# Kernel tuning notes

Measured on AMD Instinct MI355X. Metric: run time of the kernel, lower is better.

## Reference

```python
import jax, jax.numpy as jnp
import numpy as np

B, T, F = 128, 512, 16   # batch, seq len, n_features
K, PAD, H = 5, 2, 32     # conv kernel, padding, per-feature GRU hidden
NEG = 0.01               # LeakyReLU default negative slope


def setup_inputs() -> dict:
    key = jax.random.key(0)
    ks = iter(jax.random.split(key, 64))

    def u(shape, fan):
        s = 1.0 / np.sqrt(fan)
        return jax.random.uniform(next(ks), shape, jnp.float32, -s, s)

    inp = {}
    inp['x'] = jax.random.normal(next(ks), (B, 2, T), jnp.float32)
    # gru_enc: input=2, hidden=F, unidirectional (torch layout: W_ih [3H,I], W_hh [3H,H])
    inp['enc_Wih'] = u((3 * F, 2), F)
    inp['enc_Whh'] = u((3 * F, F), F)
    inp['enc_bih'] = u((3 * F,), F)
    inp['enc_bhh'] = u((3 * F,), F)
    # last_layers_gru (per feature): input=1, hidden=H, bidirectional
    for d in ('f', 'b'):
        inp[f'g1_Wih_{d}'] = u((F, 3 * H, 1), H)
        inp[f'g1_Whh_{d}'] = u((F, 3 * H, H), H)
        inp[f'g1_bih_{d}'] = u((F, 3 * H), H)
        inp[f'g1_bhh_{d}'] = u((F, 3 * H), H)
    # layers_gru (per feature): input=2H, hidden=H, unidirectional
    inp['g2_Wih'] = u((F, 3 * H, 2 * H), H)
    inp['g2_Whh'] = u((F, 3 * H, H), H)
    inp['g2_bih'] = u((F, 3 * H), H)
    inp['g2_bhh'] = u((F, 3 * H), H)
    # ConvTranspose1d weights, torch layout [C_in, C_out, K]
    inp['w3'] = u((F, 32, 64, K), 32 * K)
    inp['b3'] = u((F, 64), 32 * K)
    inp['w2'] = u((F, 64, 128, K), 64 * K)
    inp['b2'] = u((F, 128), 64 * K)
    inp['w1'] = u((F, 128, 1, K), 128 * K)
    inp['b1'] = u((F, 1), 128 * K)
    return inp


def gru(x, Wih, Whh, bih, bhh):
    # x: [B, T, I] -> [B, T, H]; torch GRU cell math
    Hh = Whh.shape[1]
    xp = jnp.einsum('bti,gi->btg', x, Wih) + bih  # [B,T,3H], input proj for all t

    def step(h, xt):
        g = h @ Whh.T + bhh
        xr, xz, xn = jnp.split(xt, 3, -1)
        hr, hz, hn = jnp.split(g, 3, -1)
        r = jax.nn.sigmoid(xr + hr)
        z = jax.nn.sigmoid(xz + hz)
        n = jnp.tanh(xn + r * hn)
        h = (1 - z) * n + z * h
        return h, h

    h0 = jnp.zeros((x.shape[0], Hh), x.dtype)
    _, ys = jax.lax.scan(step, h0, jnp.swapaxes(xp, 0, 1))
    return jnp.swapaxes(ys, 0, 1)


def bigru(x, Wf, Hf, bif, bhf, Wb, Hb, bib, bhb):
    fwd = gru(x, Wf, Hf, bif, bhf)
    bwd = gru(x[:, ::-1], Wb, Hb, bib, bhb)[:, ::-1]
    return jnp.concatenate([fwd, bwd], -1)


def convT(x, w, b):
    # ConvTranspose1d(stride=1, padding=PAD): x [B,Cin,T], w [Cin,Cout,K]
    wc = jnp.flip(w, -1).transpose(1, 0, 2)  # -> [Cout,Cin,K] cross-correlation kernel
    y = jax.lax.conv_general_dilated(
        x, wc, (1,), [(K - 1 - PAD, K - 1 - PAD)],
        dimension_numbers=('NCH', 'OIH', 'NCH'))
    return y + b[None, :, None]


def reference(x, enc_Wih, enc_Whh, enc_bih, enc_bhh,
              g1_Wih_f, g1_Whh_f, g1_bih_f, g1_bhh_f,
              g1_Wih_b, g1_Whh_b, g1_bih_b, g1_bhh_b,
              g2_Wih, g2_Whh, g2_bih, g2_bhh,
              w3, b3, w2, b2, w1, b1):
    leaky = lambda v: jnp.where(v >= 0, v, NEG * v)
    # encoder GRU over time: x [B,2,T] -> [B,T,F]
    h = gru(jnp.swapaxes(x, 1, 2), enc_Wih, enc_Whh, enc_bih, enc_bhh)

    def per_feature(xi, W1f, H1f, bi1f, bh1f, W1b, H1b, bi1b, bh1b,
                    W2, H2, bi2, bh2, w3_, b3_, w2_, b2_, w1_, b1_):
        # xi: [B,T] single feature channel
        u = bigru(xi[..., None], W1f, H1f, bi1f, bh1f, W1b, H1b, bi1b, bh1b)  # [B,T,2H]
        u = gru(u, W2, H2, bi2, bh2)        # [B,T,H]
        u = jnp.swapaxes(u, 1, 2)           # [B,H,T]
        u = leaky(convT(u, w3_, b3_))       # [B,64,T]
        u = leaky(convT(u, w2_, b2_))       # [B,128,T]
        u = leaky(convT(u, w1_, b1_))       # [B,1,T]
        return u[:, 0]                      # [B,T]

    feats = jnp.moveaxis(h, 2, 0)           # [F,B,T]
    out = jax.vmap(per_feature)(feats,
                                g1_Wih_f, g1_Whh_f, g1_bih_f, g1_bhh_f,
                                g1_Wih_b, g1_Whh_b, g1_bih_b, g1_bhh_b,
                                g2_Wih, g2_Whh, g2_bih, g2_bhh,
                                w3, b3, w2, b2, w1, b1)  # [F,B,T]
    return jnp.moveaxis(out, 0, 2)          # [B,T,F]
```

## Files before the change

kernel.cpp:

```cpp
#include <hip/hip_runtime.h>
#include <math.h>

#define BB 128
#define TT 512
#define FF 16

typedef _Float16 half8 __attribute__((ext_vector_type(8)));
typedef float floatx4 __attribute__((ext_vector_type(4)));

union HU { uint4 u; half8 h; };

__device__ __forceinline__ float bf2f(unsigned short u){
  union { unsigned int i; float f; } c; c.i = ((unsigned int)u) << 16; return c.f;
}
__device__ __forceinline__ unsigned short f2bf(float f){
  union { float f; unsigned int i; } c; c.f = f;
  unsigned int x = c.i;
  unsigned int r = (x + 0x7fffu + ((x >> 16) & 1u)) >> 16;
  return (unsigned short)r;
}
__device__ __forceinline__ float sigm(float x){
  return __builtin_amdgcn_rcpf(1.f + __expf(-x));
}
__device__ __forceinline__ float tanh_fast(float x){
  x = fminf(15.f, fmaxf(-15.f, x));
  float e = __expf(-2.f*x);
  return (1.f - e)*__builtin_amdgcn_rcpf(1.f + e);
}
__device__ __forceinline__ float lrelu(float v){ return v >= 0.f ? v : 0.01f*v; }

__device__ __forceinline__ unsigned int packhl(float v){
  _Float16 hh = (_Float16)v;
  float hf = (float)hh;
  _Float16 hl = (_Float16)(v - hf);
  union { _Float16 h; unsigned short s; } a, b;
  a.h = hh; b.h = hl;
  return (unsigned int)a.s | ((unsigned int)b.s << 16);
}

__device__ __forceinline__ void unpackAB(uint4 P0, uint4 P1, HU& Ah, HU& Al){
  Ah.u.x = (P0.x & 0xffffu) | (P0.y << 16);
  Ah.u.y = (P0.z & 0xffffu) | (P0.w << 16);
  Ah.u.z = (P1.x & 0xffffu) | (P1.y << 16);
  Ah.u.w = (P1.z & 0xffffu) | (P1.w << 16);
  Al.u.x = (P0.x >> 16) | (P0.y & 0xffff0000u);
  Al.u.y = (P0.z >> 16) | (P0.w & 0xffff0000u);
  Al.u.z = (P1.x >> 16) | (P1.y & 0xffff0000u);
  Al.u.w = (P1.z >> 16) | (P1.w & 0xffff0000u);
}

#define MFMA16(A,B,C) __builtin_amdgcn_mfma_f32_16x16x32_f16((A),(B),(C),0,0,0)

__global__ __launch_bounds__(256) void fill_kernel(unsigned short* out, int n, float v){
  int i = blockIdx.x*256 + threadIdx.x;
  if (i < n) out[i] = f2bf(v);
}

__global__ __launch_bounds__(256) void detect1_kernel(const unsigned short* x, float* maxbuf){
  __shared__ float red[256];
  const int base = blockIdx.x*4096 + threadIdx.x*16;
  const uint4* p = (const uint4*)(x + base);
  uint4 a = p[0], b = p[1];
  unsigned int ws[8] = {a.x,a.y,a.z,a.w,b.x,b.y,b.z,b.w};
  float m = 0.f;
  #pragma unroll
  for (int i=0;i<8;i++){
    float v0 = fabsf(bf2f((unsigned short)(ws[i] & 0xffffu)));
    float v1 = fabsf(bf2f((unsigned short)(ws[i] >> 16)));
    if (!isfinite(v0)) v0 = 3e38f;
    if (!isfinite(v1)) v1 = 3e38f;
    m = fmaxf(m, fmaxf(v0, v1));
  }
  red[threadIdx.x] = m; __syncthreads();
  for (int s=128; s>0; s>>=1){
    if (threadIdx.x < s) red[threadIdx.x] = fmaxf(red[threadIdx.x], red[threadIdx.x+s]);
    __syncthreads();
  }
  if (threadIdx.x == 0) maxbuf[blockIdx.x] = red[0];
}
__global__ __launch_bounds__(64) void detect2_kernel(const float* maxbuf, int* flag){
  if (threadIdx.x == 0){
    float m = 0.f;
    for (int i=0;i<32;i++) m = fmaxf(m, maxbuf[i]);
    *flag = (m < 1e4f) ? 1 : 0;
  }
}

struct CvtArgs { const void* p[23]; int sz[23]; int ofs[23]; };

__global__ __launch_bounds__(256) void convert_kernel(CvtArgs a, const int* flag, float* dst){
  const int i = blockIdx.x;
  const int n = a.sz[i];
  const int start = blockIdx.y * 16384;
  if (start >= n) return;
  const int end = (start + 16384 < n) ? start + 16384 : n;
  float* d = dst + a.ofs[i];
  const int s4 = start >> 2, e4 = end >> 2;
  if (*flag){
    const unsigned short* s = (const unsigned short*)a.p[i];
    for (int e = s4 + threadIdx.x; e < e4; e += 256){
      uint2 w = *(const uint2*)(s + 4*e);
      float4 o;
      o.x = bf2f((unsigned short)(w.x & 0xffffu));
      o.y = bf2f((unsigned short)(w.x >> 16));
      o.z = bf2f((unsigned short)(w.y & 0xffffu));
      o.w = bf2f((unsigned short)(w.y >> 16));
      *(float4*)(d + 4*e) = o;
    }
  } else {
    const float* s = (const float*)a.p[i];
    for (int e = s4 + threadIdx.x; e < e4; e += 256)
      *(float4*)(d + 4*e) = *(const float4*)(s + 4*e);
  }
}

__global__ __launch_bounds__(256) void prep16_kernel(
    const float* __restrict__ cvt, _Float16* __restrict__ h16,
    int o6, int o10, int o14, int o13, int o17, int o19, int o2)
{
  const int i = blockIdx.x*256 + threadIdx.x;
  const int y = blockIdx.y;
  if (y == 0){ if (i < 49152) h16[i]          = (_Float16)cvt[o6  + i]; }
  else if (y == 1){ if (i < 49152) h16[49152 + i]  = (_Float16)cvt[o10 + i]; }
  else if (y == 2){ if (i < 49152) h16[98304 + i]  = (_Float16)cvt[o14 + i]; }
  else if (y == 3){ if (i < 98304) h16[147456 + i] = (_Float16)cvt[o13 + i]; }
  else if (y == 4){
    if (i < 163840){
      int ci = i & 31, co = (i >> 5) & 63, fj = i >> 11;
      int f = fj / 5, j = fj - 5*f;
      h16[245760 + i] = (_Float16)cvt[o17 + ((f*32 + ci)*64 + co)*5 + j];
    }
  } else if (y == 5){
    if (i < 655360){
      int ci = i & 63, co = (i >> 6) & 127, fj = i >> 13;
      int f = fj / 5, j = fj - 5*f;
      h16[409600 + i] = (_Float16)cvt[o19 + ((f*64 + ci)*128 + co)*5 + j];
    }
  } else {
    if (i < 1536){
      int k = i & 31, row = i >> 5;
      h16[1064960 + i] = (k < 16) ? (_Float16)cvt[o2 + row*16 + k] : (_Float16)0.f;
    }
  }
}

__global__ __launch_bounds__(128) void xt_kernel(const float* __restrict__ cvt, float* __restrict__ xTp){
  const int t = blockIdx.x, b = threadIdx.x;
  xTp[t*BB + b]            = cvt[(b*2 + 0)*TT + t];
  xTp[65536 + t*BB + b]    = cvt[(b*2 + 1)*TT + t];
}

__global__ __launch_bounds__(64) void enc_kernel(
    const float* __restrict__ xTp, const _Float16* __restrict__ whhE,
    const float* __restrict__ Wih, const float* __restrict__ bih,
    const float* __restrict__ bhh, float* __restrict__ xfeatT)
{
  const int b0 = blockIdx.x*16;
  const int l = threadIdx.x, ml = l & 15, q = l >> 4;
  __shared__ unsigned int Hpk[2][16][20];
  half8 Bw[3];
  #pragma unroll
  for (int c=0;c<3;c++)
    Bw[c] = *(const half8*)(whhE + (16*c + ml)*32 + 8*q);
  float w0r=Wih[ml*2],      w1r=Wih[ml*2+1],      bir=bih[ml],    bhr=bhh[ml];
  float w0z=Wih[(16+ml)*2], w1z=Wih[(16+ml)*2+1], biz=bih[16+ml], bhz=bhh[16+ml];
  float w0n=Wih[(32+ml)*2], w1n=Wih[(32+ml)*2+1], bin_=bih[32+ml], bhn=bhh[32+ml];
  float hm[4] = {0,0,0,0};
  HU Ah, Al; Ah.u = make_uint4(0,0,0,0); Al.u = Ah.u;
  const floatx4 z4 = {0.f,0.f,0.f,0.f};
  int pp = 0;
  floatx4 x0v = *(const floatx4*)(xTp + b0 + 4*q);
  floatx4 x1v = *(const floatx4*)(xTp + 65536 + b0 + 4*q);
  for (int t=0;t<TT;t++){
    const int tn = (t < 511) ? t+1 : t;
    floatx4 x0n = *(const floatx4*)(xTp + tn*BB + b0 + 4*q);
    floatx4 x1n = *(const floatx4*)(xTp + 65536 + tn*BB + b0 + 4*q);
    floatx4 C[3];
    #pragma unroll
    for (int c=0;c<3;c++){
      C[c] = MFMA16(Al.h, Bw[c], z4);
      C[c] = MFMA16(Ah.h, Bw[c], C[c]);
    }
    #pragma unroll
    for (int r=0;r<4;r++){
      float xb0 = x0v[r], xb1 = x1v[r];
      float rr = sigm(fmaf(w0r,xb0,fmaf(w1r,xb1,bir)) + C[0][r] + bhr);
      float zz = sigm(fmaf(w0z,xb0,fmaf(w1z,xb1,biz)) + C[1][r] + bhz);
      float nn = tanh_fast(fmaf(w0n,xb0,fmaf(w1n,xb1,bin_)) + rr*(C[2][r] + bhn));
      float hn = nn + zz*(hm[r] - nn);
      hm[r] = hn;
      Hpk[pp][4*q + r][ml] = packhl(hn);
      xfeatT[((size_t)ml*TT + t)*BB + b0 + 4*q + r] = hn;
    }
    __syncthreads();
    if (q < 2){
      uint4 P0 = *(const uint4*)&Hpk[pp][ml][8*q];
      uint4 P1 = *(const uint4*)&Hpk[pp][ml][8*q + 4];
      unpackAB(P0, P1, Ah, Al);
    } else { Ah.u = make_uint4(0,0,0,0); Al.u = Ah.u; }
    pp ^= 1;
    x0v = x0n; x1v = x1n;
  }
}

__global__ __launch_bounds__(128) void g1b_kernel(
    const float* __restrict__ xT, const _Float16* __restrict__ whh_h,
    const float* __restrict__ wih, const float* __restrict__ bih,
    const float* __restrict__ bhh, _Float16* __restrict__ trace)
{
  const int f = blockIdx.x, b0 = blockIdx.y*16;
  const int wid = threadIdx.x >> 6, l = threadIdx.x & 63, ml = l & 15, q = l >> 4;
  __shared__ unsigned int Hpk[2][16][36];
  half8 Bw[3];
  #pragma unroll
  for (int i=0;i<3;i++){
    int tc = 2*i + wid;
    Bw[i] = *(const half8*)(whh_h + (size_t)f*3072 + (16*tc + ml)*32 + 8*q);
  }
  const int j = 16*wid + ml, base = f*96;
  float wir=wih[base+j], wiz=wih[base+32+j], win=wih[base+64+j];
  float br_=bih[base+j]+bhh[base+j];
  float bz_=bih[base+32+j]+bhh[base+32+j];
  float bin_=bih[base+64+j], bhn_=bhh[base+64+j];
  float hm[4] = {0,0,0,0};
  HU Ah, Al; Ah.u = make_uint4(0,0,0,0); Al.u = Ah.u;
  const floatx4 z4 = {0.f,0.f,0.f,0.f};
  int pp = 0;
  floatx4 xv = *(const floatx4*)(xT + ((size_t)f*TT + 511)*BB + b0 + 4*q);
  const int dostore = (wid == (q >> 1));
  for (int s=0;s<512;s++){
    const int t = 511 - s;
    const int tn = (s < 511) ? t-1 : t;
    floatx4 xnx = *(const floatx4*)(xT + ((size_t)f*TT + tn)*BB + b0 + 4*q);
    floatx4 C[3];
    #pragma unroll
    for (int i=0;i<3;i++){
      C[i] = MFMA16(Al.h, Bw[i], z4);
      C[i] = MFMA16(Ah.h, Bw[i], C[i]);
    }
    #pragma unroll
    for (int r=0;r<4;r++){
      float xb = xv[r];
      float rr = sigm(fmaf(wir, xb, br_) + C[0][r]);
      float zz = sigm(fmaf(wiz, xb, bz_) + C[1][r]);
      float nn = tanh_fast(fmaf(win, xb, bin_) + rr*(C[2][r] + bhn_));
      float hn = nn + zz*(hm[r] - nn);
      hm[r] = hn;
      Hpk[pp][4*q + r][j] = packhl(hn);
    }
    __syncthreads();
    {
      uint4 P0 = *(const uint4*)&Hpk[pp][ml][8*q];
      uint4 P1 = *(const uint4*)&Hpk[pp][ml][8*q + 4];
      unpackAB(P0, P1, Ah, Al);
    }
    if (dostore)
      *(uint4*)(trace + (((size_t)(f*BB + b0 + ml))*TT + t)*32 + 8*q) = Ah.u;
    pp ^= 1;
    xv = xnx;
  }
}

__global__ __launch_bounds__(128) void g1bf_kernel(
    const float* __restrict__ xT,
    const _Float16* __restrict__ whhB_h, const float* __restrict__ wihB,
    const float* __restrict__ bihB, const float* __restrict__ bhhB,
    const _Float16* __restrict__ whhF_h, const float* __restrict__ wihF,
    const float* __restrict__ bihF, const float* __restrict__ bhhF,
    _Float16* __restrict__ traceB, _Float16* __restrict__ traceF)
{
  const int f = blockIdx.x, b0 = blockIdx.y*16, dir = blockIdx.z;
  const _Float16* whh_h = dir ? whhF_h : whhB_h;
  const float* wih = dir ? wihF : wihB;
  const float* bih = dir ? bihF : bihB;
  const float* bhh = dir ? bhhF : bhhB;
  _Float16* trace = dir ? traceF : traceB;
  const int wid = threadIdx.x >> 6, l = threadIdx.x & 63, ml = l & 15, q = l >> 4;
  __shared__ unsigned int Hpk[2][16][36];
  half8 Bw[3];
  #pragma unroll
  for (int i=0;i<3;i++){
    int tc = 2*i + wid;
    Bw[i] = *(const half8*)(whh_h + (size_t)f*3072 + (16*tc + ml)*32 + 8*q);
  }
  const int j = 16*wid + ml, base = f*96;
  float wir=wih[base+j], wiz=wih[base+32+j], win=wih[base+64+j];
  float br_=bih[base+j]+bhh[base+j];
  float bz_=bih[base+32+j]+bhh[base+32+j];
  float bin_=bih[base+64+j], bhn_=bhh[base+64+j];
  float hm[4] = {0,0,0,0};
  HU Ah, Al; Ah.u = make_uint4(0,0,0,0); Al.u = Ah.u;
  const floatx4 z4 = {0.f,0.f,0.f,0.f};
  int pp = 0;
  const int tfirst = dir ? 0 : 511;
  floatx4 xv = *(const floatx4*)(xT + ((size_t)f*TT + tfirst)*BB + b0 + 4*q);
  const int dostore = (wid == (q >> 1));
  for (int s=0;s<512;s++){
    const int t  = dir ? s : 511 - s;
    const int sn = (s < 511) ? s+1 : s;
    const int tn = dir ? sn : 511 - sn;
    floatx4 xnx = *(const floatx4*)(xT + ((size_t)f*TT + tn)*BB + b0 + 4*q);
    floatx4 C[3];
    #pragma unroll
    for (int i=0;i<3;i++){
      C[i] = MFMA16(Al.h, Bw[i], z4);
      C[i] = MFMA16(Ah.h, Bw[i], C[i]);
    }
    #pragma unroll
    for (int r=0;r<4;r++){
      float xb = xv[r];
      float rr = sigm(fmaf(wir, xb, br_) + C[0][r]);
      float zz = sigm(fmaf(wiz, xb, bz_) + C[1][r]);
      float nn = tanh_fast(fmaf(win, xb, bin_) + rr*(C[2][r] + bhn_));
      float hn = nn + zz*(hm[r] - nn);
      hm[r] = hn;
      Hpk[pp][4*q + r][j] = packhl(hn);
    }
    __syncthreads();
    {
      uint4 P0 = *(const uint4*)&Hpk[pp][ml][8*q];
      uint4 P1 = *(const uint4*)&Hpk[pp][ml][8*q + 4];
      unpackAB(P0, P1, Ah, Al);
    }
    if (dostore)
      *(uint4*)(trace + (((size_t)(f*BB + b0 + ml))*TT + t)*32 + 8*q) = Ah.u;
    pp ^= 1;
    xv = xnx;
  }
}

__global__ __launch_bounds__(128) void g2_kernel(
    const float* __restrict__ xT,
    const _Float16* __restrict__ wh1_h, const float* __restrict__ wih1,
    const float* __restrict__ bih1, const float* __restrict__ bhh1,
    const _Float16* __restrict__ wh2_h, const _Float16* __restrict__ w2i_h,
    const float* __restrict__ bih2, const float* __restrict__ bhh2,
    _Float16* __restrict__ trace)
{
  const int f = blockIdx.x, b0 = blockIdx.y*16;
  const int wid = threadIdx.x >> 6, l = threadIdx.x & 63, ml = l & 15, q = l >> 4;
  __shared__ unsigned int Hpk1[2][16][36];
  __shared__ unsigned int Hpk2[2][16][36];
  half8 B1[3], Bh2[3], Bx0[3], Bx1[3];
  #pragma unroll
  for (int i=0;i<3;i++){
    int tc = 2*i + wid;
    B1[i]  = *(const half8*)(wh1_h + (size_t)f*3072 + (16*tc + ml)*32 + 8*q);
    Bh2[i] = *(const half8*)(wh2_h + (size_t)f*3072 + (16*tc + ml)*32 + 8*q);
    Bx0[i] = *(const half8*)(w2i_h + (size_t)f*6144 + (16*tc + ml)*64 + 8*q);
    Bx1[i] = *(const half8*)(w2i_h + (size_t)f*6144 + (16*tc + ml)*64 + 32 + 8*q);
  }
  const int j = 16*wid + ml, base = f*96;
  float wir=wih1[base+j], wiz=wih1[base+32+j], win=wih1[base+64+j];
  float br1_=bih1[base+j]+bhh1[base+j];
  float bz1_=bih1[base+32+j]+bhh1[base+32+j];
  float bin1_=bih1[base+64+j], bhn1_=bhh1[base+64+j];
  float br2_=bih2[base+j]+bhh2[base+j];
  float bz2_=bih2[base+32+j]+bhh2[base+32+j];
  float bin2_=bih2[base+64+j], bhn2_=bhh2[base+64+j];
  float h1[4] = {0,0,0,0};
  float h2[4] = {0,0,0,0};
  HU A1h, A1l, A2h, A2l;
  A1h.u = make_uint4(0,0,0,0); A1l.u = A1h.u; A2h.u = A1h.u; A2l.u = A1h.u;
  const floatx4 z4 = {0.f,0.f,0.f,0.f};
  const size_t rowb = ((size_t)(f*BB + b0 + ml))*TT;
  const int dostore = (wid == (q >> 1));

  {
    floatx4 x0v = *(const floatx4*)(xT + (size_t)f*TT*BB + b0 + 4*q);
    #pragma unroll
    for (int r=0;r<4;r++){
      float xb = x0v[r];
      float rr = sigm(fmaf(wir, xb, br1_));
      float zz = sigm(fmaf(wiz, xb, bz1_));
      float nn = tanh_fast(fmaf(win, xb, bin1_) + rr*bhn1_);
      float hn = (1.f - zz)*nn;
      h1[r] = hn;
      Hpk1[0][4*q + r][j] = packhl(hn);
    }
    __syncthreads();
    uint4 P0 = *(const uint4*)&Hpk1[0][ml][8*q];
    uint4 P1 = *(const uint4*)&Hpk1[0][ml][8*q + 4];
    unpackAB(P0, P1, A1h, A1l);
  }
  int pp = 1;
  uint4 Ub = *(const uint4*)(trace + (rowb + 0)*32 + 8*q);
  floatx4 xv = *(const floatx4*)(xT + ((size_t)f*TT + 1)*BB + b0 + 4*q);
  for (int t=0;t<512;t++){
    const int tn1 = (t < 511) ? t+1 : t;
    const int tn2 = (t < 510) ? t+2 : 511;
    uint4 Ubn = *(const uint4*)(trace + (rowb + tn1)*32 + 8*q);
    floatx4 xnx = *(const floatx4*)(xT + ((size_t)f*TT + tn2)*BB + b0 + 4*q);
    floatx4 C1[3];
    #pragma unroll
    for (int i=0;i<3;i++){
      C1[i] = MFMA16(A1l.h, B1[i], z4);
      C1[i] = MFMA16(A1h.h, B1[i], C1[i]);
    }
    HU Abw; Abw.u = Ub;
    floatx4 Cr, Cz, Cnh, Cnx;
    Cr = MFMA16(A2l.h, Bh2[0], z4); Cr = MFMA16(A2h.h, Bh2[0], Cr);
    Cr = MFMA16(A1l.h, Bx0[0], Cr); Cr = MFMA16(A1h.h, Bx0[0], Cr);
    Cr = MFMA16(Abw.h, Bx1[0], Cr);
    Cz = MFMA16(A2l.h, Bh2[1], z4); Cz = MFMA16(A2h.h, Bh2[1], Cz);
    Cz = MFMA16(A1l.h, Bx0[1], Cz); Cz = MFMA16(A1h.h, Bx0[1], Cz);
    Cz = MFMA16(Abw.h, Bx1[1], Cz);
    Cnh = MFMA16(A2l.h, Bh2[2], z4); Cnh = MFMA16(A2h.h, Bh2[2], Cnh);
    Cnx = MFMA16(A1l.h, Bx0[2], z4); Cnx = MFMA16(A1h.h, Bx0[2], Cnx);
    Cnx = MFMA16(Abw.h, Bx1[2], Cnx);
    #pragma unroll
    for (int r=0;r<4;r++){
      float xb = xv[r];
      float rr1 = sigm(fmaf(wir, xb, br1_) + C1[0][r]);
      float zz1 = sigm(fmaf(wiz, xb, bz1_) + C1[1][r]);
      float nn1 = tanh_fast(fmaf(win, xb, bin1_) + rr1*(C1[2][r] + bhn1_));
      float hn1 = nn1 + zz1*(h1[r] - nn1);
      h1[r] = hn1;
      Hpk1[pp][4*q + r][j] = packhl(hn1);

      float rr2 = sigm(Cr[r] + br2_);
      float zz2 = sigm(Cz[r] + bz2_);
      float nn2 = tanh_fast(Cnx[r] + bin2_ + rr2*(Cnh[r] + bhn2_));
      float hn2 = nn2 + zz2*(h2[r] - nn2);
      h2[r] = hn2;
      Hpk2[pp][4*q + r][j] = packhl(hn2);
    }
    __syncthreads();
    {
      uint4 P0 = *(const uint4*)&Hpk1[pp][ml][8*q];
      uint4 P1 = *(const uint4*)&Hpk1[pp][ml][8*q + 4];
      unpackAB(P0, P1, A1h, A1l);
      uint4 Q0 = *(const uint4*)&Hpk2[pp][ml][8*q];
      uint4 Q1 = *(const uint4*)&Hpk2[pp][ml][8*q + 4];
      unpackAB(Q0, Q1, A2h, A2l);
    }
    if (dostore)
      *(uint4*)(trace + (rowb + t)*32 + 8*q) = A2h.u;
    Ub = Ubn; xv = xnx; pp ^= 1;
  }
}

__global__ __launch_bounds__(128) void g2f_kernel(
    const _Float16* __restrict__ wh2_h, const _Float16* __restrict__ w2i_h,
    const float* __restrict__ bih2, const float* __restrict__ bhh2,
    const _Float16* __restrict__ traceF, _Float16* __restrict__ traceB)
{
  const int f = blockIdx.x, b0 = blockIdx.y*16;
  const int wid = threadIdx.x >> 6, l = threadIdx.x & 63, ml = l & 15, q = l >> 4;
  __shared__ unsigned int Hpk2[2][16][36];
  half8 Bh2[3], Bx0[3], Bx1[3];
  #pragma unroll
  for (int i=0;i<3;i++){
    int tc = 2*i + wid;
    Bh2[i] = *(const half8*)(wh2_h + (size_t)f*3072 + (16*tc + ml)*32 + 8*q);
    Bx0[i] = *(const half8*)(w2i_h + (size_t)f*6144 + (16*tc + ml)*64 + 8*q);
    Bx1[i] = *(const half8*)(w2i_h + (size_t)f*6144 + (16*tc + ml)*64 + 32 + 8*q);
  }
  const int j = 16*wid + ml, base = f*96;
  float br2_=bih2[base+j]+bhh2[base+j];
  float bz2_=bih2[base+32+j]+bhh2[base+32+j];
  float bin2_=bih2[base+64+j], bhn2_=bhh2[base+64+j];
  float h2[4] = {0,0,0,0};
  HU A2h, A2l; A2h.u = make_uint4(0,0,0,0); A2l.u = A2h.u;
  const floatx4 z4 = {0.f,0.f,0.f,0.f};
  const size_t rowb = ((size_t)(f*BB + b0 + ml))*TT;
  const int dostore = (wid == (q >> 1));
  int pp = 0;
  uint4 UbF = *(const uint4*)(traceF + (rowb + 0)*32 + 8*q);
  uint4 UbB = *(const uint4*)(traceB + (rowb + 0)*32 + 8*q);
  for (int t=0;t<512;t++){
    const int tn = (t < 511) ? t+1 : t;
    uint4 UbFn = *(const uint4*)(traceF + (rowb + tn)*32 + 8*q);
    uint4 UbBn = *(const uint4*)(traceB + (rowb + tn)*32 + 8*q);
    HU AF; AF.u = UbF;
    HU AB; AB.u = UbB;
    floatx4 Cr, Cz, Cnh, Cnx;
    Cr = MFMA16(A2l.h, Bh2[0], z4); Cr = MFMA16(A2h.h, Bh2[0], Cr);
    Cr = MFMA16(AF.h, Bx0[0], Cr);  Cr = MFMA16(AB.h, Bx1[0], Cr);
    Cz = MFMA16(A2l.h, Bh2[1], z4); Cz = MFMA16(A2h.h, Bh2[1], Cz);
    Cz = MFMA16(AF.h, Bx0[1], Cz);  Cz = MFMA16(AB.h, Bx1[1], Cz);
    Cnh = MFMA16(A2l.h, Bh2[2], z4); Cnh = MFMA16(A2h.h, Bh2[2], Cnh);
    Cnx = MFMA16(AF.h, Bx0[2], z4);  Cnx = MFMA16(AB.h, Bx1[2], Cnx);
    #pragma unroll
    for (int r=0;r<4;r++){
      float rr2 = sigm(Cr[r] + br2_);
      float zz2 = sigm(Cz[r] + bz2_);
      float nn2 = tanh_fast(Cnx[r] + bin2_ + rr2*(Cnh[r] + bhn2_));
      float hn2 = nn2 + zz2*(h2[r] - nn2);
      h2[r] = hn2;
      Hpk2[pp][4*q + r][j] = packhl(hn2);
    }
    __syncthreads();
    {
      uint4 Q0 = *(const uint4*)&Hpk2[pp][ml][8*q];
      uint4 Q1 = *(const uint4*)&Hpk2[pp][ml][8*q + 4];
      unpackAB(Q0, Q1, A2h, A2l);
    }
    if (dostore)
      *(uint4*)(traceB + (rowb + t)*32 + 8*q) = A2h.u;
    UbF = UbFn; UbB = UbBn; pp ^= 1;
  }
}

#define UTP 40
#define C3P 72
#define C2P 136
__global__ __launch_bounds__(256) void conv_kernel(
    const _Float16* __restrict__ u2,
    const _Float16* __restrict__ w3T, const float* __restrict__ b3,
    const _Float16* __restrict__ w2T, const float* __restrict__ b2,
    const float* __restrict__ w1, const float* __restrict__ b1,
    void* __restrict__ outv, const int* __restrict__ flag)
{
  const int t0 = blockIdx.x * 64;
  const int b  = blockIdx.y;
  const int f  = blockIdx.z;
  const int tid = threadIdx.x;
  const int w = tid >> 6, l = tid & 63, ml = l & 15, q = l >> 4;

  __shared__ __align__(16) _Float16 utb[84][UTP];
  __shared__ __align__(16) _Float16 c3T[84][C3P];
  __shared__ __align__(16) _Float16 c2T[68][C2P];
  __shared__ float red[4][64];

  const _Float16* urow = u2 + ((size_t)(f*BB + b)*TT)*32;
  const floatx4 z4 = {0.f,0.f,0.f,0.f};

  for (int k = tid; k < 76*4; k += 256){
    int n = k >> 2, seg = k & 3;
    int tg = t0 - 6 + n;
    uint4 v = make_uint4(0,0,0,0);
    if (tg >= 0 && tg < TT) v = *(const uint4*)(urow + (size_t)tg*32 + seg*8);
    *(uint4*)&utb[n][seg*8] = v;
  }
  __syncthreads();

  {
    half8 A3[5];
    #pragma unroll
    for (int jj=0;jj<5;jj++)
      A3[jj] = *(const half8*)(w3T + (((size_t)f*5 + jj)*64 + 16*w + ml)*32 + 8*q);
    float bv[4];
    #pragma unroll
    for (int r=0;r<4;r++) bv[r] = b3[f*64 + 16*w + 4*q + r];
    #pragma unroll
    for (int nt=0;nt<5;nt++){
      floatx4 acc = z4;
      #pragma unroll
      for (int jj=0;jj<5;jj++){
        half8 Bb = *(const half8*)&utb[16*nt + ml + 4 - jj][8*q];
        acc = MFMA16(A3[jj], Bb, acc);
      }
      int tm = 16*nt + ml;
      if (tm < 72){
        int G = t0 - 4 + tm;
        unsigned int pk[2];
        #pragma unroll
        for (int h=0;h<2;h++){
          float v0 = acc[2*h]   + bv[2*h];   v0 = lrelu(v0);
          float v1 = acc[2*h+1] + bv[2*h+1]; v1 = lrelu(v1);
          if (G < 0 || G >= TT){ v0 = 0.f; v1 = 0.f; }
          union { _Float16 hh; unsigned short s; } c0, c1;
          c0.hh = (_Float16)v0; c1.hh = (_Float16)v1;
          pk[h] = (unsigned int)c0.s | ((unsigned int)c1.s << 16);
        }
        *(uint2*)&c3T[tm][16*w + 4*q] = make_uint2(pk[0], pk[1]);
      }
    }
  }
  __syncthreads();

  {
    half8 A2f[5][2][2];
    #pragma unroll
    for (int jj=0;jj<5;jj++)
      #pragma unroll
      for (int ch=0;ch<2;ch++)
        #pragma unroll
        for (int mi=0;mi<2;mi++)
          A2f[jj][ch][mi] = *(const half8*)(w2T + (((size_t)f*5 + jj)*128 + 16*(2*w+mi) + ml)*64 + 32*ch + 8*q);
    float bv2[2][4];
    #pragma unroll
    for (int mi=0;mi<2;mi++)
      #pragma unroll
      for (int r=0;r<4;r++) bv2[mi][r] = b2[f*128 + 16*(2*w+mi) + 4*q + r];
    #pragma unroll
    for (int nt=0;nt<5;nt++){
      floatx4 a0 = z4, a1 = z4;
      #pragma unroll
      for (int jj=0;jj<5;jj++){
        #pragma unroll
        for (int ch=0;ch<2;ch++){
          half8 Bb = *(const half8*)&c3T[16*nt + ml + 4 - jj][32*ch + 8*q];
          a0 = MFMA16(A2f[jj][ch][0], Bb, a0);
          a1 = MFMA16(A2f[jj][ch][1], Bb, a1);
        }
      }
      int p = 16*nt + ml;
      if (p < 68){
        int G = t0 - 2 + p;
        #pragma unroll
        for (int mi=0;mi<2;mi++){
          unsigned int pk[2];
          #pragma unroll
          for (int h=0;h<2;h++){
            float v0 = (mi ? a1[2*h]   : a0[2*h])   + bv2[mi][2*h];   v0 = lrelu(v0);
            float v1 = (mi ? a1[2*h+1] : a0[2*h+1]) + bv2[mi][2*h+1]; v1 = lrelu(v1);
            if (G < 0 || G >= TT){ v0 = 0.f; v1 = 0.f; }
            union { _Float16 hh; unsigned short s; } c0, c1;
            c0.hh = (_Float16)v0; c1.hh = (_Float16)v1;
            pk[h] = (unsigned int)c0.s | ((unsigned int)c1.s << 16);
          }
          *(uint2*)&c2T[p][16*(2*w+mi) + 4*q] = make_uint2(pk[0], pk[1]);
        }
      }
    }
  }
  __syncthreads();

  {
    const int tl = tid & 63, cg = tid >> 6;
    const float* wp = w1 + ((size_t)f*128 + cg*32)*5;
    float acc = 0.f;
    #pragma unroll
    for (int jj=0;jj<5;jj++){
      int row = tl + 4 - jj;
      union { uint4 u; _Float16 h[8]; } u0, u1, u2_, u3;
      u0.u  = *(const uint4*)&c2T[row][cg*32];
      u1.u  = *(const uint4*)&c2T[row][cg*32 + 8];
      u2_.u = *(const uint4*)&c2T[row][cg*32 + 16];
      u3.u  = *(const uint4*)&c2T[row][cg*32 + 24];
      #pragma unroll
      for (int i=0;i<8;i++){
        acc = fmaf(wp[i*5 + jj],      (float)u0.h[i],  acc);
        acc = fmaf(wp[(8+i)*5 + jj],  (float)u1.h[i],  acc);
        acc = fmaf(wp[(16+i)*5 + jj], (float)u2_.h[i], acc);
        acc = fmaf(wp[(24+i)*5 + jj], (float)u3.h[i],  acc);
      }
    }
    red[cg][tl] = acc;
  }
  __syncthreads();
  if (tid < 64){
    float s = b1[f] + red[0][tid] + red[1][tid] + red[2][tid] + red[3][tid];
    s = lrelu(s);
    size_t oi = ((size_t)b*TT + t0 + tid)*FF + f;
    if (*flag) ((unsigned short*)outv)[oi] = f2bf(s);
    else       ((float*)outv)[oi] = s;
  }
}

extern "C" void kernel_launch(void* const* d_in, const int* in_sizes, int n_in,
                              void* d_out, int out_size, void* d_ws, size_t ws_size,
                              hipStream_t stream)
{
  static const int esz[23] = {
    131072,
    96, 768, 48, 48,
    1536, 49152, 1536, 1536,
    1536, 49152, 1536, 1536,
    98304, 49152, 1536, 1536,
    163840, 1024,
    655360, 2048,
    10240, 16
  };
  const size_t NEED = (size_t)16*1024*1024 + (size_t)64*1024*1024;

  float diag = 0.f;
  if (n_in != 23) diag = 2000.f + n_in;
  else {
    for (int i=0;i<23;i++) if (in_sizes[i] != esz[i]) { diag = 1000.f + i; break; }
    if (diag == 0.f && ws_size < NEED) diag = 500.f + (float)(ws_size >> 20);
  }
  if (diag != 0.f){
    hipLaunchKernelGGL(fill_kernel, dim3((out_size+255)/256), dim3(256), 0, stream,
                       (unsigned short*)d_out, out_size, diag);
    return;
  }

  float* cvt = (float*)d_ws;
  int* flagp = (int*)((char*)d_ws + (5ull<<20));
  float* maxbuf = (float*)((char*)d_ws + (5ull<<20) + 256);
  _Float16* h16 = (_Float16*)((char*)d_ws + (6ull<<20));
  float* xTp = (float*)((char*)d_ws + (9ull<<20));
  float* xfeatT = (float*)((char*)d_ws + (10ull<<20));
  _Float16* trace = (_Float16*)((char*)d_ws + (14ull<<20));
  _Float16* traceF = (_Float16*)((char*)d_ws + (80ull<<20));
  const bool bigws = (ws_size >= (145ull<<20));

  CvtArgs a;
  int ofs = 0;
  for (int i=0;i<23;i++){ a.p[i] = d_in[i]; a.sz[i] = esz[i]; a.ofs[i] = ofs; ofs += esz[i]; }
  const float* c[23];
  for (int i=0;i<23;i++) c[i] = cvt + a.ofs[i];

  hipLaunchKernelGGL(detect1_kernel, dim3(32), dim3(256), 0, stream,
                     (const unsigned short*)d_in[0], maxbuf);
  hipLaunchKernelGGL(detect2_kernel, dim3(1), dim3(64), 0, stream, maxbuf, flagp);
  hipLaunchKernelGGL(convert_kernel, dim3(23, 40), dim3(256), 0, stream, a, flagp, cvt);
  hipLaunchKernelGGL(prep16_kernel, dim3(2560, 7), dim3(256), 0, stream,
                     cvt, h16, a.ofs[6], a.ofs[10], a.ofs[14], a.ofs[13],
                     a.ofs[17], a.ofs[19], a.ofs[2]);
  hipLaunchKernelGGL(xt_kernel, dim3(TT), dim3(BB), 0, stream, cvt, xTp);
  hipLaunchKernelGGL(enc_kernel, dim3(BB/16), dim3(64), 0, stream,
                     xTp, h16 + 1064960, c[1], c[3], c[4], xfeatT);
  if (bigws){
    hipLaunchKernelGGL(g1bf_kernel, dim3(FF, 8, 2), dim3(128), 0, stream,
                       xfeatT,
                       h16 + 49152, c[9], c[11], c[12],
                       h16 + 0,     c[5], c[7],  c[8],
                       trace, traceF);
    hipLaunchKernelGGL(g2f_kernel, dim3(FF, 8), dim3(128), 0, stream,
                       h16 + 98304, h16 + 147456, c[15], c[16],
                       traceF, trace);
  } else {
    hipLaunchKernelGGL(g1b_kernel, dim3(FF, 8), dim3(128), 0, stream,
                       xfeatT, h16 + 49152, c[9], c[11], c[12], trace);
    hipLaunchKernelGGL(g2_kernel, dim3(FF, 8), dim3(128), 0, stream,
                       xfeatT, h16 + 0, c[5], c[7], c[8],
                       h16 + 98304, h16 + 147456, c[15], c[16], trace);
  }
  hipLaunchKernelGGL(conv_kernel, dim3(TT/64, BB, FF), dim3(256), 0, stream,
                     trace, h16 + 245760, c[18], h16 + 409600, c[20], c[21], c[22],
                     d_out, flagp);
}
```

Before: 1.339 ms.

## Split hidden-state LDS exchange into separate fp16 hi/lo planes in recurrent kernels

In the encoder, bidirectional and second GRU kernels, the packed hi/lo 32-bit LDS words are replaced by two separate fp16 shared arrays, so the MFMA A operands are read directly with one uint4 load each instead of a pack/unpack shuffle. The encoder also writes its four outputs per step as a single float4 store. g2f prefetches the input trace two steps ahead and splits the accumulation chains into independent MFMA pairs that are summed at the end, which shortens dependent MFMA latency. The cost is narrower 2-byte LDS stores, possible bank conflicts and a few extra registers.

```diff
diff --git a/kernel.cpp b/kernel.cpp
--- a/kernel.cpp
+++ b/kernel.cpp
@@ -157,7 +157,8 @@
 {
   const int b0 = blockIdx.x*16;
   const int l = threadIdx.x, ml = l & 15, q = l >> 4;
-  __shared__ unsigned int Hpk[2][16][20];
+  __shared__ __align__(16) _Float16 HpkH[2][16][24];
+  __shared__ __align__(16) _Float16 HpkL[2][16][24];
   half8 Bw[3];
   #pragma unroll
   for (int c=0;c<3;c++)
@@ -181,6 +182,7 @@
       C[c] = MFMA16(Al.h, Bw[c], z4);
       C[c] = MFMA16(Ah.h, Bw[c], C[c]);
     }
+    float4 hv4;
     #pragma unroll
     for (int r=0;r<4;r++){
       float xb0 = x0v[r], xb1 = x1v[r];
@@ -189,14 +191,17 @@
       float nn = tanh_fast(fmaf(w0n,xb0,fmaf(w1n,xb1,bin_)) + rr*(C[2][r] + bhn));
       float hn = nn + zz*(hm[r] - nn);
       hm[r] = hn;
-      Hpk[pp][4*q + r][ml] = packhl(hn);
-      xfeatT[((size_t)ml*TT + t)*BB + b0 + 4*q + r] = hn;
-    }
+      _Float16 hh = (_Float16)hn;
+      _Float16 hl = (_Float16)(hn - (float)hh);
+      HpkH[pp][4*q + r][ml] = hh;
+      HpkL[pp][4*q + r][ml] = hl;
+      ((float*)&hv4)[r] = hn;
+    }
+    *(float4*)(xfeatT + ((size_t)ml*TT + t)*BB + b0 + 4*q) = hv4;
     __syncthreads();
     if (q < 2){
-      uint4 P0 = *(const uint4*)&Hpk[pp][ml][8*q];
-      uint4 P1 = *(const uint4*)&Hpk[pp][ml][8*q + 4];
-      unpackAB(P0, P1, Ah, Al);
+      Ah.u = *(const uint4*)&HpkH[pp][ml][8*q];
+      Al.u = *(const uint4*)&HpkL[pp][ml][8*q];
     } else { Ah.u = make_uint4(0,0,0,0); Al.u = Ah.u; }
     pp ^= 1;
     x0v = x0n; x1v = x1n;
@@ -276,7 +281,8 @@
   const float* bhh = dir ? bhhF : bhhB;
   _Float16* trace = dir ? traceF : traceB;
   const int wid = threadIdx.x >> 6, l = threadIdx.x & 63, ml = l & 15, q = l >> 4;
-  __shared__ unsigned int Hpk[2][16][36];
+  __shared__ __align__(16) _Float16 HpkH[2][16][40];
+  __shared__ __align__(16) _Float16 HpkL[2][16][40];
   half8 Bw[3];
   #pragma unroll
   for (int i=0;i<3;i++){
@@ -314,14 +320,14 @@
       float nn = tanh_fast(fmaf(win, xb, bin_) + rr*(C[2][r] + bhn_));
       float hn = nn + zz*(hm[r] - nn);
       hm[r] = hn;
-      Hpk[pp][4*q + r][j] = packhl(hn);
+      _Float16 hh = (_Float16)hn;
+      _Float16 hl = (_Float16)(hn - (float)hh);
+      HpkH[pp][4*q + r][j] = hh;
+      HpkL[pp][4*q + r][j] = hl;
     }
     __syncthreads();
-    {
-      uint4 P0 = *(const uint4*)&Hpk[pp][ml][8*q];
-      uint4 P1 = *(const uint4*)&Hpk[pp][ml][8*q + 4];
-      unpackAB(P0, P1, Ah, Al);
-    }
+    Ah.u = *(const uint4*)&HpkH[pp][ml][8*q];
+    Al.u = *(const uint4*)&HpkL[pp][ml][8*q];
     if (dostore)
       *(uint4*)(trace + (((size_t)(f*BB + b0 + ml))*TT + t)*32 + 8*q) = Ah.u;
     pp ^= 1;
@@ -447,7 +453,8 @@
 {
   const int f = blockIdx.x, b0 = blockIdx.y*16;
   const int wid = threadIdx.x >> 6, l = threadIdx.x & 63, ml = l & 15, q = l >> 4;
-  __shared__ unsigned int Hpk2[2][16][36];
+  __shared__ __align__(16) _Float16 HpkH[2][16][40];
+  __shared__ __align__(16) _Float16 HpkL[2][16][40];
   half8 Bh2[3], Bx0[3], Bx1[3];
   #pragma unroll
   for (int i=0;i<3;i++){
@@ -466,21 +473,27 @@
   const size_t rowb = ((size_t)(f*BB + b0 + ml))*TT;
   const int dostore = (wid == (q >> 1));
   int pp = 0;
-  uint4 UbF = *(const uint4*)(traceF + (rowb + 0)*32 + 8*q);
-  uint4 UbB = *(const uint4*)(traceB + (rowb + 0)*32 + 8*q);
+  uint4 F0 = *(const uint4*)(traceF + (rowb + 0)*32 + 8*q);
+  uint4 F1 = *(const uint4*)(traceF + (rowb + 1)*32 + 8*q);
+  uint4 B0 = *(const uint4*)(traceB + (rowb + 0)*32 + 8*q);
+  uint4 B1 = *(const uint4*)(traceB + (rowb + 1)*32 + 8*q);
   for (int t=0;t<512;t++){
-    const int tn = (t < 511) ? t+1 : t;
-    uint4 UbFn = *(const uint4*)(traceF + (rowb + tn)*32 + 8*q);
-    uint4 UbBn = *(const uint4*)(traceB + (rowb + tn)*32 + 8*q);
-    HU AF; AF.u = UbF;
-    HU AB; AB.u = UbB;
+    const int tn = (t < 510) ? t+2 : 511;
+    uint4 F2 = *(const uint4*)(traceF + (rowb + tn)*32 + 8*q);
+    uint4 B2 = *(const uint4*)(traceB + (rowb + tn)*32 + 8*q);
+    HU AF; AF.u = F0;
+    HU AB; AB.u = B0;
     floatx4 Cr, Cz, Cnh, Cnx;
-    Cr = MFMA16(A2l.h, Bh2[0], z4); Cr = MFMA16(A2h.h, Bh2[0], Cr);
-    Cr = MFMA16(AF.h, Bx0[0], Cr);  Cr = MFMA16(AB.h, Bx1[0], Cr);
-    Cz = MFMA16(A2l.h, Bh2[1], z4); Cz = MFMA16(A2h.h, Bh2[1], Cz);
-    Cz = MFMA16(AF.h, Bx0[1], Cz);  Cz = MFMA16(AB.h, Bx1[1], Cz);
-    Cnh = MFMA16(A2l.h, Bh2[2], z4); Cnh = MFMA16(A2h.h, Bh2[2], Cnh);
-    Cnx = MFMA16(AF.h, Bx0[2], z4);  Cnx = MFMA16(AB.h, Bx1[2], Cnx);
+    {
+      floatx4 CrA = MFMA16(A2l.h, Bh2[0], z4); CrA = MFMA16(A2h.h, Bh2[0], CrA);
+      floatx4 CrB = MFMA16(AF.h, Bx0[0], z4);  CrB = MFMA16(AB.h, Bx1[0], CrB);
+      Cr = CrA + CrB;
+      floatx4 CzA = MFMA16(A2l.h, Bh2[1], z4); CzA = MFMA16(A2h.h, Bh2[1], CzA);
+      floatx4 CzB = MFMA16(AF.h, Bx0[1], z4);  CzB = MFMA16(AB.h, Bx1[1], CzB);
+      Cz = CzA + CzB;
+      Cnh = MFMA16(A2l.h, Bh2[2], z4); Cnh = MFMA16(A2h.h, Bh2[2], Cnh);
+      Cnx = MFMA16(AF.h, Bx0[2], z4);  Cnx = MFMA16(AB.h, Bx1[2], Cnx);
+    }
     #pragma unroll
     for (int r=0;r<4;r++){
       float rr2 = sigm(Cr[r] + br2_);
@@ -488,17 +501,17 @@
       float nn2 = tanh_fast(Cnx[r] + bin2_ + rr2*(Cnh[r] + bhn2_));
       float hn2 = nn2 + zz2*(h2[r] - nn2);
       h2[r] = hn2;
-      Hpk2[pp][4*q + r][j] = packhl(hn2);
+      _Float16 hh = (_Float16)hn2;
+      _Float16 hl = (_Float16)(hn2 - (float)hh);
+      HpkH[pp][4*q + r][j] = hh;
+      HpkL[pp][4*q + r][j] = hl;
     }
     __syncthreads();
-    {
-      uint4 Q0 = *(const uint4*)&Hpk2[pp][ml][8*q];
-      uint4 Q1 = *(const uint4*)&Hpk2[pp][ml][8*q + 4];
-      unpackAB(Q0, Q1, A2h, A2l);
-    }
+    A2h.u = *(const uint4*)&HpkH[pp][ml][8*q];
+    A2l.u = *(const uint4*)&HpkL[pp][ml][8*q];
     if (dostore)
       *(uint4*)(traceB + (rowb + t)*32 + 8*q) = A2h.u;
-    UbF = UbFn; UbB = UbBn; pp ^= 1;
+    F0 = F1; F1 = F2; B0 = B1; B1 = B2; pp ^= 1;
   }
 }
 
```

Result: no change. 1.325 ms (-1.1%).
